# Performance work log

Hardware: AMD Instinct MI355X
Metric: run time of the kernel (lower is better)

Reference implementation:

```python
import jax, jax.numpy as jnp
import numpy as np

SIG = [1, 1, 1, 1, -1]  # Cl(4,1)
NVEC = 5
GA = 1 << NVEC  # 32


def _build_gp_table():
    # Cayley table for the geometric product on blades indexed by bitmask.
    G = np.zeros((GA, GA, GA), np.float32)
    for a in range(GA):
        for b in range(GA):
            s = 0
            t = a >> 1
            while t:
                s += bin(t & b).count('1')
                t >>= 1
            sign = -1.0 if (s & 1) else 1.0
            common = a & b
            for i in range(NVEC):
                if (common >> i) & 1:
                    sign *= SIG[i]
            G[a, b, a ^ b] = sign
    return G

GP_TABLE = jnp.asarray(_build_gp_table())


def geometric_product(x, y):
    return jnp.einsum('...i,...j,ijk->...k', x, y, GP_TABLE)


def manifold_norm(x):
    # normalize each multivector onto the unit sphere in R^32
    return x / (jnp.linalg.norm(x, axis=-1, keepdims=True) + 1e-6)


def versor_linear(x, W, b):
    # channel mixing shared across multivector components: x [..., in, ga]
    return jnp.einsum('...ig,oi->...og', x, W) + b


def layer_norm2d(x, w, b):
    # LayerNorm over last two dims [D, ga] jointly
    mu = jnp.mean(x, axis=(-2, -1), keepdims=True)
    var = jnp.var(x, axis=(-2, -1), keepdims=True)
    return (x - mu) / jnp.sqrt(var + 1e-5) * w + b


def attention(x, Wq, bq, Wk, bk, Wv, bv, Wo, bo, n_heads):
    B, S, D, G = x.shape
    dh = D // n_heads
    q = versor_linear(x, Wq, bq).reshape(B, S, n_heads, dh, G)
    k = versor_linear(x, Wk, bk).reshape(B, S, n_heads, dh, G)
    v = versor_linear(x, Wv, bv).reshape(B, S, n_heads, dh, G)
    scale = 1.0 / np.sqrt(dh * G).astype(np.float32)
    scores = jnp.einsum('bshdg,bthdg->bhst', q, k) * scale
    probs = jax.nn.softmax(scores, axis=-1)
    o = jnp.einsum('bhst,bthdg->bshdg', probs, v).reshape(B, S, D, G)
    return versor_linear(o, Wo, bo)


N_HEADS = 8


def forward(x, Wq, bq, Wk, bk, Wv, bv, Wo, bo, ln1_w, ln1_b, ln2_w, ln2_b,
            gamma1, gamma2, W1, b1, W2, b2, Wr, br, Wc, bc):
    L = Wq.shape[0]
    for l in range(L):
        h = attention(layer_norm2d(x, ln1_w[l], ln1_b[l]),
                      Wq[l], bq[l], Wk[l], bk[l], Wv[l], bv[l], Wo[l], bo[l], N_HEADS)
        x = manifold_norm(x + gamma1[l] * h)
        m = versor_linear(layer_norm2d(x, ln2_w[l], ln2_b[l]), W1[l], b1[l])
        m = versor_linear(jnp.tanh(m), W2[l], b2[l])
        x = manifold_norm(x + gamma2[l] * m)
    # RecursiveRotorAccumulator: log(S)-step inclusive scan of rotors
    delta = versor_linear(x, Wr, br)
    rot = 0.5 * delta
    rot = rot.at[..., 0].add(1.0)
    rot = manifold_norm(rot)
    S = x.shape[1]
    step = 1
    while step < S:
        left = rot[:, :-step]
        right = rot[:, step:]
        comb = manifold_norm(geometric_product(right, left))
        rot = jnp.concatenate([rot[:, :step], comb], axis=1)
        step *= 2
    pooled = rot[:, -1]  # [B, D, ga]
    logits = pooled.reshape(pooled.shape[0], -1) @ Wc.T + bc
    return logits


def setup_inputs() -> dict:
    key = jax.random.key(0)
    B, S, D, G, L, NC = 8, 256, 64, GA, 4, 1000
    E = 4 * D  # expansion hidden
    ks = jax.random.split(key, 16)
    sd = 0.02
    inp = {
        'x': jax.random.normal(ks[0], (B, S, D, G), jnp.float32),
        'Wq': jax.random.normal(ks[1], (L, D, D), jnp.float32) * sd,
        'bq': jnp.zeros((L, D, G), jnp.float32),
        'Wk': jax.random.normal(ks[2], (L, D, D), jnp.float32) * sd,
        'bk': jnp.zeros((L, D, G), jnp.float32),
        'Wv': jax.random.normal(ks[3], (L, D, D), jnp.float32) * sd,
        'bv': jnp.zeros((L, D, G), jnp.float32),
        'Wo': jax.random.normal(ks[4], (L, D, D), jnp.float32) * sd,
        'bo': jnp.zeros((L, D, G), jnp.float32),
        'ln1_w': jnp.ones((L, D, G), jnp.float32),
        'ln1_b': jnp.zeros((L, D, G), jnp.float32),
        'ln2_w': jnp.ones((L, D, G), jnp.float32),
        'ln2_b': jnp.zeros((L, D, G), jnp.float32),
        'gamma1': 1e-5 * jnp.ones((L, D, G), jnp.float32),
        'gamma2': 1e-5 * jnp.ones((L, D, G), jnp.float32),
        'W1': jax.random.normal(ks[5], (L, E, D), jnp.float32) * sd,
        'b1': jnp.zeros((L, E, G), jnp.float32),
        'W2': jax.random.normal(ks[6], (L, D, E), jnp.float32) * sd,
        'b2': jnp.zeros((L, D, G), jnp.float32),
        'Wr': jax.random.normal(ks[7], (D, D), jnp.float32) * sd,
        'br': jnp.zeros((D, G), jnp.float32),
        'Wc': jax.random.normal(ks[8], (NC, D * G), jnp.float32) * sd,
        'bc': jnp.zeros((NC,), jnp.float32),
    }
    return inp


def reference(x, Wq, bq, Wk, bk, Wv, bv, Wo, bo, ln1_w, ln1_b, ln2_w, ln2_b,
              gamma1, gamma2, W1, b1, W2, b2, Wr, br, Wc, bc):
    return forward(x, Wq, bq, Wk, bk, Wv, bv, Wo, bo, ln1_w, ln1_b, ln2_w, ln2_b,
                   gamma1, gamma2, W1, b1, W2, b2, Wr, br, Wc, bc)
```

## Files before the change

kernel.cpp:

```cpp
#include <hip/hip_runtime.h>
#include <hip/hip_bf16.h>

constexpr int kB  = 8;
constexpr int kS  = 256;
constexpr int kD  = 64;
constexpr int kG  = 32;
constexpr int kE  = 256;
constexpr int kNH = 8;
constexpr int kHD = 256;
constexpr int kDG = kD * kG;
constexpr int kT  = kB * kS;
constexpr int kNC = 1000;

using bf16x8 = __attribute__((ext_vector_type(8))) short;
using f32x4  = __attribute__((ext_vector_type(4))) float;

__device__ __forceinline__ short f2bf(float f) {
    unsigned u = __float_as_uint(f);
    unsigned r = (u + 0x7FFFu + ((u >> 16) & 1u)) >> 16;
    return (short)r;
}

__device__ __forceinline__ float tanh_fast(float x) {
    float a = fabsf(x);
    float e = __expf(-2.f * a);
    float t = (1.f - e) / (1.f + e);
    return copysignf(t, x);
}

__global__ __launch_bounds__(256) void ln_kernel(const float* __restrict__ Xin,
                                                 const float* __restrict__ w,
                                                 const float* __restrict__ b,
                                                 float* __restrict__ A) {
    int t = blockIdx.x, tid = threadIdx.x;
    const float* xp = Xin + (size_t)t * kDG;
    __shared__ float r1[256], r2[256];
    float v[8], s = 0.f, ss = 0.f;
#pragma unroll
    for (int j = 0; j < 8; j++) {
        float x = xp[tid + j * 256];
        v[j] = x; s += x; ss += x * x;
    }
    r1[tid] = s; r2[tid] = ss; __syncthreads();
    for (int o = 128; o > 0; o >>= 1) {
        if (tid < o) { r1[tid] += r1[tid + o]; r2[tid] += r2[tid + o]; }
        __syncthreads();
    }
    float mean = r1[0] * (1.f / kDG);
    float var  = r2[0] * (1.f / kDG) - mean * mean;
    float rstd = rsqrtf(var + 1e-5f);
    float* ao = A + (size_t)t * kDG;
#pragma unroll
    for (int j = 0; j < 8; j++) {
        int jj = tid + j * 256;
        ao[jj] = (v[j] - mean) * rstd * w[jj] + b[jj];
    }
}

__device__ __forceinline__ void epi_res_mn_ln(
    const f32x4 (&acc)[4][2], const float* __restrict__ bias,
    const float* __restrict__ Xin, float* __restrict__ Xout,
    const float* __restrict__ gamma,
    const float* __restrict__ lnw, const float* __restrict__ lnb,
    float* __restrict__ Aout, int tok, int l16, int quad, bool do_ln) {
    const size_t tb = (size_t)tok * kDG;
    float xv[4][2][4];
    float s = 0.f, ss = 0.f;
#pragma unroll
    for (int mt = 0; mt < 4; ++mt)
#pragma unroll
        for (int r = 0; r < 4; ++r) {
            int o = mt * 16 + quad * 4 + r;
            float vv[2]; float sq = 0.f;
#pragma unroll
            for (int nt = 0; nt < 2; ++nt) {
                int g = nt * 16 + l16;
                float h = acc[mt][nt][r] + bias[o * kG + g];
                float v = Xin[tb + o * kG + g] + gamma[o * kG + g] * h;
                vv[nt] = v; sq = fmaf(v, v, sq);
            }
#pragma unroll
            for (int off = 1; off < 16; off <<= 1) sq += __shfl_xor(sq, off, 64);
            float rn = 1.f / (sqrtf(sq) + 1e-6f);
#pragma unroll
            for (int nt = 0; nt < 2; ++nt) {
                int g = nt * 16 + l16;
                float x = vv[nt] * rn;
                xv[mt][nt][r] = x;
                Xout[tb + o * kG + g] = x;
                s += x; ss = fmaf(x, x, ss);
            }
        }
    if (!do_ln) return;
#pragma unroll
    for (int off = 1; off < 64; off <<= 1) {
        s += __shfl_xor(s, off, 64); ss += __shfl_xor(ss, off, 64);
    }
    float mean = s * (1.f / kDG);
    float var  = ss * (1.f / kDG) - mean * mean;
    float rstd = rsqrtf(var + 1e-5f);
#pragma unroll
    for (int mt = 0; mt < 4; ++mt)
#pragma unroll
        for (int nt = 0; nt < 2; ++nt) {
            int g = nt * 16 + l16;
#pragma unroll
            for (int r = 0; r < 4; ++r) {
                int o = mt * 16 + quad * 4 + r;
                Aout[tb + o * kG + g] = (xv[mt][nt][r] - mean) * rstd * lnw[o * kG + g] + lnb[o * kG + g];
            }
        }
}

__global__ __launch_bounds__(256) void vlinT_kernel(const float* __restrict__ X,
                                                    const float* __restrict__ W,
                                                    const float* __restrict__ bias,
                                                    float* __restrict__ OutT) {
    __shared__ float sx[kDG];
    __shared__ float sw[kD * kD];
    int t = blockIdx.x, tid = threadIdx.x;
    const float* xp = X + (size_t)t * kDG;
    for (int j = tid; j < kDG; j += 256) sx[j] = xp[j];
    for (int j = tid; j < kD * kD; j += 256) sw[j] = W[j];
    __syncthreads();
    int g = tid & 31, ob = tid >> 5;
    int b = t >> 8, s = t & 255;
    float* op = OutT + ((size_t)b * kD * kS + s) * kG;
    for (int o = ob; o < kD; o += 8) {
        float acc = bias[o * kG + g];
        const float* wr = sw + o * kD;
#pragma unroll
        for (int i = 0; i < kD; i++) acc += wr[i] * sx[i * kG + g];
        op[(size_t)o * kS * kG + g] = acc;
    }
}

__global__ __launch_bounds__(256, 2) void mlp1_kernel(
    const float* __restrict__ X, const float* __restrict__ W,
    const float* __restrict__ bias, unsigned short* __restrict__ outH) {
    constexpr int M = 256;
    constexpr int WS = 64 + 8;
    __shared__ short sW[M * WS];
    __shared__ short sXT[4][32][WS];

    const int tid = threadIdx.x, wave = tid >> 6, lane = tid & 63;
    const int l16 = lane & 15, quad = lane >> 4;
    const int tok = blockIdx.x * 4 + wave;

    for (int j = tid * 4; j < M * 64; j += 1024) {
        const float4 w4 = *(const float4*)(W + j);
        int o = j >> 6, i = j & 63;
        *(short4*)&sW[o * WS + i] = make_short4(f2bf(w4.x), f2bf(w4.y), f2bf(w4.z), f2bf(w4.w));
    }
    {
        const int g4 = (lane & 7) * 4;
        const int i0 = (lane >> 3) * 8;
        const float* xp = X + (size_t)tok * kDG;
#pragma unroll
        for (int half = 0; half < 2; ++half) {
            float4 vr[4];
#pragma unroll
            for (int r = 0; r < 4; ++r)
                vr[r] = *(const float4*)(xp + (i0 + half * 4 + r) * kG + g4);
#pragma unroll
            for (int gg = 0; gg < 4; ++gg)
                *(short4*)&sXT[wave][g4 + gg][i0 + half * 4] =
                    make_short4(f2bf((&vr[0].x)[gg]), f2bf((&vr[1].x)[gg]),
                                f2bf((&vr[2].x)[gg]), f2bf((&vr[3].x)[gg]));
        }
    }
    __syncthreads();

    bf16x8 bfr[2][2];
#pragma unroll
    for (int c = 0; c < 2; ++c)
#pragma unroll
        for (int nt = 0; nt < 2; ++nt)
            bfr[c][nt] = *(const bf16x8*)&sXT[wave][nt * 16 + l16][c * 32 + quad * 8];

    f32x4 acc[16][2];
#pragma unroll
    for (int mt = 0; mt < 16; ++mt)
#pragma unroll
        for (int nt = 0; nt < 2; ++nt) acc[mt][nt] = (f32x4){0.f, 0.f, 0.f, 0.f};

#pragma unroll
    for (int mt = 0; mt < 16; ++mt)
#pragma unroll
        for (int c = 0; c < 2; ++c) {
            bf16x8 afr = *(const bf16x8*)&sW[(mt * 16 + l16) * WS + c * 32 + quad * 8];
#pragma unroll
            for (int nt = 0; nt < 2; ++nt)
                acc[mt][nt] = __builtin_amdgcn_mfma_f32_16x16x32_bf16(afr, bfr[c][nt], acc[mt][nt], 0, 0, 0);
        }

    unsigned short* op = outH + (size_t)tok * M * kG;
#pragma unroll
    for (int mt = 0; mt < 16; ++mt)
#pragma unroll
        for (int nt = 0; nt < 2; ++nt) {
            int g = nt * 16 + l16;
            int e0 = mt * 16 + quad * 4;
            short4 s4;
            s4.x = f2bf(tanh_fast(acc[mt][nt][0] + bias[(e0 + 0) * kG + g]));
            s4.y = f2bf(tanh_fast(acc[mt][nt][1] + bias[(e0 + 1) * kG + g]));
            s4.z = f2bf(tanh_fast(acc[mt][nt][2] + bias[(e0 + 2) * kG + g]));
            s4.w = f2bf(tanh_fast(acc[mt][nt][3] + bias[(e0 + 3) * kG + g]));
            *(short4*)&op[g * M + e0] = s4;
        }
}

__global__ __launch_bounds__(256, 2) void gemmWo_fused_kernel(
    const float* __restrict__ X, const float* __restrict__ W,
    const float* __restrict__ bias,
    const float* __restrict__ Xin, const float* __restrict__ gamma,
    const float* __restrict__ lnw, const float* __restrict__ lnb,
    float* __restrict__ Xout, float* __restrict__ Aout) {
    constexpr int WS = 64 + 8;
    __shared__ short sW[64 * WS];
    __shared__ short sXT[4][32][WS];

    const int tid = threadIdx.x, wave = tid >> 6, lane = tid & 63;
    const int l16 = lane & 15, quad = lane >> 4;
    const int tok = blockIdx.x * 4 + wave;

    for (int j = tid * 4; j < 64 * 64; j += 1024) {
        const float4 w4 = *(const float4*)(W + j);
        int o = j >> 6, i = j & 63;
        *(short4*)&sW[o * WS + i] = make_short4(f2bf(w4.x), f2bf(w4.y), f2bf(w4.z), f2bf(w4.w));
    }
    {
        const int g4 = (lane & 7) * 4;
        const int i0 = (lane >> 3) * 8;
        const float* xp = X + (size_t)tok * kDG;
#pragma unroll
        for (int half = 0; half < 2; ++half) {
            float4 vr[4];
#pragma unroll
            for (int r = 0; r < 4; ++r)
                vr[r] = *(const float4*)(xp + (i0 + half * 4 + r) * kG + g4);
#pragma unroll
            for (int gg = 0; gg < 4; ++gg)
                *(short4*)&sXT[wave][g4 + gg][i0 + half * 4] =
                    make_short4(f2bf((&vr[0].x)[gg]), f2bf((&vr[1].x)[gg]),
                                f2bf((&vr[2].x)[gg]), f2bf((&vr[3].x)[gg]));
        }
    }
    __syncthreads();

    bf16x8 bfr[2][2];
#pragma unroll
    for (int c = 0; c < 2; ++c)
#pragma unroll
        for (int nt = 0; nt < 2; ++nt)
            bfr[c][nt] = *(const bf16x8*)&sXT[wave][nt * 16 + l16][c * 32 + quad * 8];

    f32x4 acc[4][2];
#pragma unroll
    for (int mt = 0; mt < 4; ++mt)
#pragma unroll
        for (int nt = 0; nt < 2; ++nt) acc[mt][nt] = (f32x4){0.f, 0.f, 0.f, 0.f};

#pragma unroll
    for (int mt = 0; mt < 4; ++mt)
#pragma unroll
        for (int c = 0; c < 2; ++c) {
            bf16x8 afr = *(const bf16x8*)&sW[(mt * 16 + l16) * WS + c * 32 + quad * 8];
#pragma unroll
            for (int nt = 0; nt < 2; ++nt)
                acc[mt][nt] = __builtin_amdgcn_mfma_f32_16x16x32_bf16(afr, bfr[c][nt], acc[mt][nt], 0, 0, 0);
        }

    epi_res_mn_ln(acc, bias, Xin, Xout, gamma, lnw, lnb, Aout, tok, l16, quad, true);
}

__global__ __launch_bounds__(256, 2) void gemm_qkv_kernel(
    const float* __restrict__ X,
    const float* __restrict__ Wq, const float* __restrict__ Wk, const float* __restrict__ Wv,
    const float* __restrict__ bq, const float* __restrict__ bk, const float* __restrict__ bv,
    unsigned short* __restrict__ Q, unsigned short* __restrict__ K, unsigned short* __restrict__ V) {
    constexpr int WS = 64 + 8;
    __shared__ short sW[3 * 64 * WS];
    __shared__ short sXT[4][32][WS];

    const int tid = threadIdx.x, wave = tid >> 6, lane = tid & 63;
    const int l16 = lane & 15, quad = lane >> 4;
    const int tok = blockIdx.x * 4 + wave;

    const float* Wp[3] = {Wq, Wk, Wv};
#pragma unroll
    for (int w = 0; w < 3; ++w)
        for (int j = tid * 4; j < 64 * 64; j += 1024) {
            const float4 w4 = *(const float4*)(Wp[w] + j);
            int o = j >> 6, i = j & 63;
            *(short4*)&sW[w * 64 * WS + o * WS + i] =
                make_short4(f2bf(w4.x), f2bf(w4.y), f2bf(w4.z), f2bf(w4.w));
        }
    {
        const int g4 = (lane & 7) * 4;
        const int i0 = (lane >> 3) * 8;
        const float* xp = X + (size_t)tok * kDG;
#pragma unroll
        for (int half = 0; half < 2; ++half) {
            float4 vr[4];
#pragma unroll
            for (int r = 0; r < 4; ++r)
                vr[r] = *(const float4*)(xp + (i0 + half * 4 + r) * kG + g4);
#pragma unroll
            for (int gg = 0; gg < 4; ++gg)
                *(short4*)&sXT[wave][g4 + gg][i0 + half * 4] =
                    make_short4(f2bf((&vr[0].x)[gg]), f2bf((&vr[1].x)[gg]),
                                f2bf((&vr[2].x)[gg]), f2bf((&vr[3].x)[gg]));
        }
    }
    __syncthreads();

    bf16x8 bfr[2][2];
#pragma unroll
    for (int c = 0; c < 2; ++c)
#pragma unroll
        for (int nt = 0; nt < 2; ++nt)
            bfr[c][nt] = *(const bf16x8*)&sXT[wave][nt * 16 + l16][c * 32 + quad * 8];

    f32x4 acc[3][4][2];
#pragma unroll
    for (int w = 0; w < 3; ++w)
#pragma unroll
        for (int mt = 0; mt < 4; ++mt)
#pragma unroll
            for (int nt = 0; nt < 2; ++nt) acc[w][mt][nt] = (f32x4){0.f, 0.f, 0.f, 0.f};

#pragma unroll
    for (int w = 0; w < 3; ++w)
#pragma unroll
        for (int mt = 0; mt < 4; ++mt)
#pragma unroll
            for (int c = 0; c < 2; ++c) {
                bf16x8 afr = *(const bf16x8*)&sW[w * 64 * WS + (mt * 16 + l16) * WS + c * 32 + quad * 8];
#pragma unroll
                for (int nt = 0; nt < 2; ++nt)
                    acc[w][mt][nt] = __builtin_amdgcn_mfma_f32_16x16x32_bf16(afr, bfr[c][nt], acc[w][mt][nt], 0, 0, 0);
            }

    unsigned short* Op[3] = {Q, K, V};
    const float* Bp[3] = {bq, bk, bv};
#pragma unroll
    for (int w = 0; w < 3; ++w) {
        unsigned short* op = Op[w] + (size_t)tok * kDG;
#pragma unroll
        for (int mt = 0; mt < 4; ++mt)
#pragma unroll
            for (int nt = 0; nt < 2; ++nt) {
                int g = nt * 16 + l16;
#pragma unroll
                for (int r = 0; r < 4; ++r) {
                    int o = mt * 16 + quad * 4 + r;
                    op[o * kG + g] = (unsigned short)f2bf(acc[w][mt][nt][r] + Bp[w][o * kG + g]);
                }
            }
    }
}

template<bool DO_LN>
__global__ __launch_bounds__(256, 2) void mlp2_fused_kernel(
    const unsigned short* __restrict__ Mb,
    const float* __restrict__ W2, const float* __restrict__ b2,
    float* __restrict__ X, const float* __restrict__ gamma,
    const float* __restrict__ lnw, const float* __restrict__ lnb,
    float* __restrict__ Aout) {
    constexpr int WS = 256 + 8;
    __shared__ short sW[64 * WS];
    const int tid = threadIdx.x, wave = tid >> 6, lane = tid & 63;
    const int l16 = lane & 15, quad = lane >> 4;
    const int tok = blockIdx.x * 4 + wave;

    for (int j = tid * 4; j < 64 * 256; j += 1024) {
        const float4 w4 = *(const float4*)(W2 + j);
        int o = j >> 8, i = j & 255;
        *(short4*)&sW[o * WS + i] = make_short4(f2bf(w4.x), f2bf(w4.y), f2bf(w4.z), f2bf(w4.w));
    }
    __syncthreads();

    f32x4 acc[4][2];
#pragma unroll
    for (int mt = 0; mt < 4; ++mt)
#pragma unroll
        for (int nt = 0; nt < 2; ++nt) acc[mt][nt] = (f32x4){0.f, 0.f, 0.f, 0.f};

    const unsigned short* mp = Mb + (size_t)tok * kG * kE;
#pragma unroll
    for (int c = 0; c < 8; ++c) {
        bf16x8 bfr[2];
#pragma unroll
        for (int nt = 0; nt < 2; ++nt)
            bfr[nt] = *(const bf16x8*)&mp[(nt * 16 + l16) * kE + c * 32 + quad * 8];
#pragma unroll
        for (int mt = 0; mt < 4; ++mt) {
            bf16x8 afr = *(const bf16x8*)&sW[(mt * 16 + l16) * WS + c * 32 + quad * 8];
#pragma unroll
            for (int nt = 0; nt < 2; ++nt)
                acc[mt][nt] = __builtin_amdgcn_mfma_f32_16x16x32_bf16(afr, bfr[nt], acc[mt][nt], 0, 0, 0);
        }
    }

    epi_res_mn_ln(acc, b2, X, X, gamma, lnw, lnb, Aout, tok, l16, quad, DO_LN);
}

constexpr int QSTR = 264;
constexpr int VSTR = 40;

__global__ __launch_bounds__(256) void attn_mfma_kernel(const unsigned short* __restrict__ Q,
                                                        const unsigned short* __restrict__ K,
                                                        const unsigned short* __restrict__ V,
                                                        float* __restrict__ O) {
    __shared__ short sQ[64 * QSTR];
    __shared__ short sKV[256 * VSTR];

    const int qt = blockIdx.x, h = blockIdx.y, b = blockIdx.z;
    const int tid = threadIdx.x;
    const int wave = tid >> 6, lane = tid & 63;
    const int l16 = lane & 15, quad = lane >> 4;

    const size_t bh = (size_t)b * kS * kDG + (size_t)h * kHD;

#pragma unroll
    for (int it = 0; it < 8; ++it) {
        int j = it * 2048 + tid * 8;
        int row = j >> 8, col = j & 255;
        *(bf16x8*)&sQ[row * QSTR + col] =
            *(const bf16x8*)(Q + bh + (size_t)(qt * 64 + row) * kDG + col);
    }
    __syncthreads();

    bf16x8 afrag[8];
    {
        int row = wave * 16 + l16;
#pragma unroll
        for (int c = 0; c < 8; ++c)
            afrag[c] = *(const bf16x8*)&sQ[row * QSTR + c * 32 + quad * 8];
    }

    f32x4 acc[16];
#pragma unroll
    for (int i = 0; i < 16; ++i) acc[i] = (f32x4){0.f, 0.f, 0.f, 0.f};

    for (int kt = 0; kt < 8; ++kt) {
        __syncthreads();
#pragma unroll
        for (int it = 0; it < 4; ++it) {
            int j = it * 2048 + tid * 8;
            int row = j >> 8, col = j & 255;
            *(bf16x8*)&sKV[row * QSTR + col] =
                *(const bf16x8*)(K + bh + (size_t)(kt * 32 + row) * kDG + col);
        }
        __syncthreads();
#pragma unroll
        for (int nt = 0; nt < 2; ++nt) {
            int key = nt * 16 + l16;
            f32x4 a = acc[kt * 2 + nt];
#pragma unroll
            for (int c = 0; c < 8; ++c) {
                bf16x8 bfrag = *(const bf16x8*)&sKV[key * QSTR + c * 32 + quad * 8];
                a = __builtin_amdgcn_mfma_f32_16x16x32_bf16(afrag[c], bfrag, a, 0, 0, 0);
            }
            acc[kt * 2 + nt] = a;
        }
    }
    __syncthreads();

    float inv[4];
#pragma unroll
    for (int r = 0; r < 4; ++r) {
        float m = -1e30f;
#pragma unroll
        for (int t = 0; t < 16; ++t) m = fmaxf(m, acc[t][r]);
#pragma unroll
        for (int off = 1; off < 16; off <<= 1) m = fmaxf(m, __shfl_xor(m, off, 16));
        float s = 0.f;
#pragma unroll
        for (int t = 0; t < 16; ++t) {
            float p = __expf((acc[t][r] - m) * 0.0625f);
            acc[t][r] = p; s += p;
        }
#pragma unroll
        for (int off = 1; off < 16; off <<= 1) s += __shfl_xor(s, off, 16);
        inv[r] = 1.f / s;
    }

#pragma unroll
    for (int t = 0; t < 16; ++t)
#pragma unroll
        for (int r = 0; r < 4; ++r)
            sQ[(wave * 16 + quad * 4 + r) * QSTR + t * 16 + l16] = f2bf(acc[t][r]);

    f32x4 oacc[16];
#pragma unroll
    for (int i = 0; i < 16; ++i) oacc[i] = (f32x4){0.f, 0.f, 0.f, 0.f};

    for (int vt = 0; vt < 8; ++vt) {
        __syncthreads();
        {
            int kb = tid >> 5;
#pragma unroll
            for (int it = 0; it < 2; ++it) {
                int db = (tid & 31) + it * 32;
                short4 vr[4];
#pragma unroll
                for (int r = 0; r < 4; ++r)
                    vr[r] = *(const short4*)(V + bh + (size_t)(vt * 32 + kb * 4 + r) * kDG + db * 4);
#pragma unroll
                for (int i = 0; i < 4; ++i) {
                    short4 p = make_short4((&vr[0].x)[i], (&vr[1].x)[i],
                                           (&vr[2].x)[i], (&vr[3].x)[i]);
                    *(short4*)&sKV[(db * 4 + i) * VSTR + kb * 4] = p;
                }
            }
        }
        __syncthreads();
        bf16x8 pfrag = *(const bf16x8*)&sQ[(wave * 16 + l16) * QSTR + vt * 32 + quad * 8];
#pragma unroll
        for (int dt = 0; dt < 16; ++dt) {
            bf16x8 vfrag = *(const bf16x8*)&sKV[(dt * 16 + l16) * VSTR + quad * 8];
            oacc[dt] = __builtin_amdgcn_mfma_f32_16x16x32_bf16(pfrag, vfrag, oacc[dt], 0, 0, 0);
        }
    }

    {
        int qrow = qt * 64 + wave * 16 + quad * 4;
#pragma unroll
        for (int dt = 0; dt < 16; ++dt)
#pragma unroll
            for (int r = 0; r < 4; ++r)
                O[bh + (size_t)(qrow + r) * kDG + dt * 16 + l16] = oacc[dt][r] * inv[r];
    }
}

constexpr int pc_ce(unsigned v) { int c = 0; while (v) { c += v & 1; v >>= 1; } return c; }
constexpr unsigned gp_mask_ce(int a) {
    unsigned m = 0;
    for (int c = 0; c < 32; ++c) {
        int b = a ^ c;
        int s = (a & b) >> 4;
        for (int t = a >> 1; t; t >>= 1) s += pc_ce(t & b);
        if (s & 1) m |= (1u << c);
    }
    return m;
}

template<int A>
__device__ __forceinline__ void gp_term(const float* x, const float* y, float* acc) {
    constexpr unsigned m = gp_mask_ce(A);
    const float xa = x[A], nxa = -xa;
#pragma unroll
    for (int c = 0; c < 32; ++c)
        acc[c] = fmaf(((m >> c) & 1u) ? nxa : xa, y[A ^ c], acc[c]);
}

__device__ __forceinline__ void gp_mn_t(const float* x, const float* y, float* out) {
    float acc[32];
#pragma unroll
    for (int c = 0; c < 32; ++c) acc[c] = 0.f;
    gp_term<0>(x, y, acc);  gp_term<1>(x, y, acc);  gp_term<2>(x, y, acc);  gp_term<3>(x, y, acc);
    gp_term<4>(x, y, acc);  gp_term<5>(x, y, acc);  gp_term<6>(x, y, acc);  gp_term<7>(x, y, acc);
    gp_term<8>(x, y, acc);  gp_term<9>(x, y, acc);  gp_term<10>(x, y, acc); gp_term<11>(x, y, acc);
    gp_term<12>(x, y, acc); gp_term<13>(x, y, acc); gp_term<14>(x, y, acc); gp_term<15>(x, y, acc);
    gp_term<16>(x, y, acc); gp_term<17>(x, y, acc); gp_term<18>(x, y, acc); gp_term<19>(x, y, acc);
    gp_term<20>(x, y, acc); gp_term<21>(x, y, acc); gp_term<22>(x, y, acc); gp_term<23>(x, y, acc);
    gp_term<24>(x, y, acc); gp_term<25>(x, y, acc); gp_term<26>(x, y, acc); gp_term<27>(x, y, acc);
    gp_term<28>(x, y, acc); gp_term<29>(x, y, acc); gp_term<30>(x, y, acc); gp_term<31>(x, y, acc);
    float ss = 0.f;
#pragma unroll
    for (int c = 0; c < 32; ++c) ss = fmaf(acc[c], acc[c], ss);
    float r = 1.f / (sqrtf(ss) + 1e-6f);
#pragma unroll
    for (int c = 0; c < 32; ++c) out[c] = acc[c] * r;
}

__device__ __forceinline__ void leaf_load(const float* base, float* v) {
#pragma unroll
    for (int i = 0; i < 8; ++i) {
        const float4 f = *(const float4*)(base + i * 4);
        v[i * 4 + 0] = 0.5f * f.x; v[i * 4 + 1] = 0.5f * f.y;
        v[i * 4 + 2] = 0.5f * f.z; v[i * 4 + 3] = 0.5f * f.w;
    }
    v[0] += 1.f;
    float ss = 0.f;
#pragma unroll
    for (int c = 0; c < 32; ++c) ss = fmaf(v[c], v[c], ss);
    float r = 1.f / (sqrtf(ss) + 1e-6f);
#pragma unroll
    for (int c = 0; c < 32; ++c) v[c] *= r;
}

__global__ __launch_bounds__(256) void scanreg_kernel(const float* __restrict__ DT,
                                                      float* __restrict__ pooled) {
    const int wave = threadIdx.x >> 6, lane = threadIdx.x & 63;
    const int seq = blockIdx.x * 4 + wave;
    const float* base = DT + ((size_t)seq * kS + lane * 4) * kG;

    float R[32], Y[32], P[32], Xa[32], Yb[32];

    leaf_load(base, R);
    for (int j = 1; j < 4; ++j) {
        leaf_load(base + j * kG, Y);
        gp_mn_t(Y, R, R);
    }

    for (int step = 1; step < 64; step <<= 1) {
        const bool up = lane & step;
#pragma unroll
        for (int c = 0; c < 32; ++c) P[c] = __shfl_xor(R[c], step, 64);
#pragma unroll
        for (int c = 0; c < 32; ++c) {
            Xa[c] = up ? R[c] : P[c];
            Yb[c] = up ? P[c] : R[c];
        }
        gp_mn_t(Xa, Yb, R);
    }

    if (lane == 0) {
        float* op = pooled + (size_t)seq * kG;
#pragma unroll
        for (int i = 0; i < 8; ++i)
            *(float4*)(op + i * 4) = make_float4(R[i * 4], R[i * 4 + 1], R[i * 4 + 2], R[i * 4 + 3]);
    }
}

__global__ __launch_bounds__(256) void cls2_kernel(const float* __restrict__ P,
                                                   const float* __restrict__ Wc,
                                                   const float* __restrict__ bc,
                                                   float* __restrict__ out) {
    __shared__ float sp[kB * kDG];
    const int tid = threadIdx.x, wave = tid >> 6, lane = tid & 63;
    for (int j = tid * 4; j < kB * kDG; j += 1024)
        *(float4*)&sp[j] = *(const float4*)(P + j);
    __syncthreads();

    const int c = blockIdx.x * 4 + wave;
    const float* w = Wc + (size_t)c * kDG;
    float acc[kB];
#pragma unroll
    for (int b = 0; b < kB; ++b) acc[b] = 0.f;
#pragma unroll
    for (int cc = 0; cc < 8; ++cc) {
        const float4 w4 = *(const float4*)(w + cc * 256 + lane * 4);
#pragma unroll
        for (int b = 0; b < kB; ++b) {
            const float4 p4 = *(const float4*)&sp[b * kDG + cc * 256 + lane * 4];
            acc[b] += w4.x * p4.x + w4.y * p4.y + w4.z * p4.z + w4.w * p4.w;
        }
    }
#pragma unroll
    for (int b = 0; b < kB; ++b)
#pragma unroll
        for (int off = 32; off > 0; off >>= 1) acc[b] += __shfl_xor(acc[b], off, 64);
    if (lane == 0) {
        float bias = bc[c];
#pragma unroll
        for (int b = 0; b < kB; ++b) out[b * kNC + c] = acc[b] + bias;
    }
}

extern "C" void kernel_launch(void* const* d_in, const int* in_sizes, int n_in,
                              void* d_out, int out_size, void* d_ws, size_t ws_size,
                              hipStream_t stream) {
    const float* x_in = (const float*)d_in[0];
    const float* Wq   = (const float*)d_in[1];
    const float* bq   = (const float*)d_in[2];
    const float* Wk   = (const float*)d_in[3];
    const float* bk   = (const float*)d_in[4];
    const float* Wv   = (const float*)d_in[5];
    const float* bv   = (const float*)d_in[6];
    const float* Wo   = (const float*)d_in[7];
    const float* bo   = (const float*)d_in[8];
    const float* ln1w = (const float*)d_in[9];
    const float* ln1b = (const float*)d_in[10];
    const float* ln2w = (const float*)d_in[11];
    const float* ln2b = (const float*)d_in[12];
    const float* gm1  = (const float*)d_in[13];
    const float* gm2  = (const float*)d_in[14];
    const float* W1   = (const float*)d_in[15];
    const float* b1   = (const float*)d_in[16];
    const float* W2   = (const float*)d_in[17];
    const float* b2   = (const float*)d_in[18];
    const float* Wr   = (const float*)d_in[19];
    const float* br   = (const float*)d_in[20];
    const float* Wc   = (const float*)d_in[21];
    const float* bc   = (const float*)d_in[22];

    const size_t NEL = (size_t)kT * kDG;
    float* F  = (float*)d_ws;
    float* X  = F;
    float* A  = F + NEL;
    float* Qb = F + 2 * NEL;
    float* Kb = F + 3 * NEL;
    float* Vb = F + 4 * NEL;
    unsigned short* Qh = (unsigned short*)Qb;
    unsigned short* Kh = (unsigned short*)Kb;
    unsigned short* Vh = (unsigned short*)Vb;
    unsigned short* Mb = (unsigned short*)Kb;
    float* pooled = Qb;

    ln_kernel<<<kT, 256, 0, stream>>>(x_in, ln1w, ln1b, A);

    for (int l = 0; l < 4; l++) {
        gemm_qkv_kernel<<<kT / 4, 256, 0, stream>>>(A,
            Wq + l * kD * kD, Wk + l * kD * kD, Wv + l * kD * kD,
            bq + l * kDG, bk + l * kDG, bv + l * kDG, Qh, Kh, Vh);
        attn_mfma_kernel<<<dim3(4, kNH, kB), 256, 0, stream>>>(Qh, Kh, Vh, A);
        gemmWo_fused_kernel<<<kT / 4, 256, 0, stream>>>(A, Wo + l * kD * kD, bo + l * kDG,
            l == 0 ? x_in : X, gm1 + l * kDG, ln2w + l * kDG, ln2b + l * kDG, X, A);
        mlp1_kernel<<<kT / 4, 256, 0, stream>>>(A, W1 + l * kE * kD, b1 + l * kE * kG, Mb);
        if (l < 3)
            mlp2_fused_kernel<true><<<kT / 4, 256, 0, stream>>>(Mb, W2 + l * kD * kE, b2 + l * kDG,
                X, gm2 + l * kDG, ln1w + (l + 1) * kDG, ln1b + (l + 1) * kDG, A);
        else
            mlp2_fused_kernel<false><<<kT / 4, 256, 0, stream>>>(Mb, W2 + l * kD * kE, b2 + l * kDG,
                X, gm2 + l * kDG, nullptr, nullptr, nullptr);
    }

    vlinT_kernel<<<kT, 256, 0, stream>>>(X, Wr, br, A);
    scanreg_kernel<<<kB * kD / 4, 256, 0, stream>>>(A, pooled);
    cls2_kernel<<<kNC / 4, 256, 0, stream>>>(pooled, Wc, bc, (float*)d_out);
}
```

Measured before the change: 610.6 us.

## Pre-convert weights to bf16 once and register-prefetch K/V tiles in attention

Adds a single up-front kernel that converts all layer weights (Wq, Wk, Wv, Wo, W1, W2) to bf16 in a workspace buffer. Each GEMM block then copies ready-made bf16 weights into shared memory instead of re-reading fp32 and converting in every one of the 512 blocks per launch. In the attention kernel, the next K and V tile is loaded into registers while the current tile is being computed, and barriers are rearranged to overlap global loads with MFMA work. This raises register pressure and uses extra workspace memory.

```diff
diff --git a/kernel.cpp b/kernel.cpp
--- a/kernel.cpp
+++ b/kernel.cpp
@@ -26,6 +26,23 @@
     float e = __expf(-2.f * a);
     float t = (1.f - e) / (1.f + e);
     return copysignf(t, x);
+}
+
+__global__ __launch_bounds__(256) void cvtw_kernel(
+    const float* __restrict__ Wq, const float* __restrict__ Wk,
+    const float* __restrict__ Wv, const float* __restrict__ Wo,
+    const float* __restrict__ W1, const float* __restrict__ W2,
+    unsigned short* __restrict__ dst) {
+    int idx = (blockIdx.x * 256 + threadIdx.x) * 4;
+    const float* src; int off;
+    if      (idx <  16384) { src = Wq; off = 0; }
+    else if (idx <  32768) { src = Wk; off = 16384; }
+    else if (idx <  49152) { src = Wv; off = 32768; }
+    else if (idx <  65536) { src = Wo; off = 49152; }
+    else if (idx < 131072) { src = W1; off = 65536; }
+    else                   { src = W2; off = 131072; }
+    const float4 v = *(const float4*)(src + (idx - off));
+    *(short4*)&dst[idx] = make_short4(f2bf(v.x), f2bf(v.y), f2bf(v.z), f2bf(v.w));
 }
 
 __global__ __launch_bounds__(256) void ln_kernel(const float* __restrict__ Xin,
@@ -136,7 +153,7 @@
 }
 
 __global__ __launch_bounds__(256, 2) void mlp1_kernel(
-    const float* __restrict__ X, const float* __restrict__ W,
+    const float* __restrict__ X, const unsigned short* __restrict__ Wh,
     const float* __restrict__ bias, unsigned short* __restrict__ outH) {
     constexpr int M = 256;
     constexpr int WS = 64 + 8;
@@ -147,10 +164,9 @@
     const int l16 = lane & 15, quad = lane >> 4;
     const int tok = blockIdx.x * 4 + wave;
 
-    for (int j = tid * 4; j < M * 64; j += 1024) {
-        const float4 w4 = *(const float4*)(W + j);
+    for (int j = tid * 8; j < M * 64; j += 2048) {
         int o = j >> 6, i = j & 63;
-        *(short4*)&sW[o * WS + i] = make_short4(f2bf(w4.x), f2bf(w4.y), f2bf(w4.z), f2bf(w4.w));
+        *(bf16x8*)&sW[o * WS + i] = *(const bf16x8*)(Wh + j);
     }
     {
         const int g4 = (lane & 7) * 4;
@@ -211,7 +227,7 @@
 }
 
 __global__ __launch_bounds__(256, 2) void gemmWo_fused_kernel(
-    const float* __restrict__ X, const float* __restrict__ W,
+    const float* __restrict__ X, const unsigned short* __restrict__ Wh,
     const float* __restrict__ bias,
     const float* __restrict__ Xin, const float* __restrict__ gamma,
     const float* __restrict__ lnw, const float* __restrict__ lnb,
@@ -224,10 +240,9 @@
     const int l16 = lane & 15, quad = lane >> 4;
     const int tok = blockIdx.x * 4 + wave;
 
-    for (int j = tid * 4; j < 64 * 64; j += 1024) {
-        const float4 w4 = *(const float4*)(W + j);
+    for (int j = tid * 8; j < 64 * 64; j += 2048) {
         int o = j >> 6, i = j & 63;
-        *(short4*)&sW[o * WS + i] = make_short4(f2bf(w4.x), f2bf(w4.y), f2bf(w4.z), f2bf(w4.w));
+        *(bf16x8*)&sW[o * WS + i] = *(const bf16x8*)(Wh + j);
     }
     {
         const int g4 = (lane & 7) * 4;
@@ -276,7 +291,8 @@
 
 __global__ __launch_bounds__(256, 2) void gemm_qkv_kernel(
     const float* __restrict__ X,
-    const float* __restrict__ Wq, const float* __restrict__ Wk, const float* __restrict__ Wv,
+    const unsigned short* __restrict__ Wqh, const unsigned short* __restrict__ Wkh,
+    const unsigned short* __restrict__ Wvh,
     const float* __restrict__ bq, const float* __restrict__ bk, const float* __restrict__ bv,
     unsigned short* __restrict__ Q, unsigned short* __restrict__ K, unsigned short* __restrict__ V) {
     constexpr int WS = 64 + 8;
@@ -287,14 +303,12 @@
     const int l16 = lane & 15, quad = lane >> 4;
     const int tok = blockIdx.x * 4 + wave;
 
-    const float* Wp[3] = {Wq, Wk, Wv};
+    const unsigned short* Wp[3] = {Wqh, Wkh, Wvh};
 #pragma unroll
     for (int w = 0; w < 3; ++w)
-        for (int j = tid * 4; j < 64 * 64; j += 1024) {
-            const float4 w4 = *(const float4*)(Wp[w] + j);
+        for (int j = tid * 8; j < 64 * 64; j += 2048) {
             int o = j >> 6, i = j & 63;
-            *(short4*)&sW[w * 64 * WS + o * WS + i] =
-                make_short4(f2bf(w4.x), f2bf(w4.y), f2bf(w4.z), f2bf(w4.w));
+            *(bf16x8*)&sW[w * 64 * WS + o * WS + i] = *(const bf16x8*)(Wp[w] + j);
         }
     {
         const int g4 = (lane & 7) * 4;
@@ -364,7 +378,7 @@
 template<bool DO_LN>
 __global__ __launch_bounds__(256, 2) void mlp2_fused_kernel(
     const unsigned short* __restrict__ Mb,
-    const float* __restrict__ W2, const float* __restrict__ b2,
+    const unsigned short* __restrict__ W2h, const float* __restrict__ b2,
     float* __restrict__ X, const float* __restrict__ gamma,
     const float* __restrict__ lnw, const float* __restrict__ lnb,
     float* __restrict__ Aout) {
@@ -374,10 +388,9 @@
     const int l16 = lane & 15, quad = lane >> 4;
     const int tok = blockIdx.x * 4 + wave;
 
-    for (int j = tid * 4; j < 64 * 256; j += 1024) {
-        const float4 w4 = *(const float4*)(W2 + j);
+    for (int j = tid * 8; j < 64 * 256; j += 2048) {
         int o = j >> 8, i = j & 255;
-        *(short4*)&sW[o * WS + i] = make_short4(f2bf(w4.x), f2bf(w4.y), f2bf(w4.z), f2bf(w4.w));
+        *(bf16x8*)&sW[o * WS + i] = *(const bf16x8*)(W2h + j);
     }
     __syncthreads();
 
@@ -430,6 +443,13 @@
         *(bf16x8*)&sQ[row * QSTR + col] =
             *(const bf16x8*)(Q + bh + (size_t)(qt * 64 + row) * kDG + col);
     }
+    bf16x8 kpre[4];
+#pragma unroll
+    for (int it = 0; it < 4; ++it) {
+        int j = it * 2048 + tid * 8;
+        int row = j >> 8, col = j & 255;
+        kpre[it] = *(const bf16x8*)(K + bh + (size_t)row * kDG + col);
+    }
     __syncthreads();
 
     bf16x8 afrag[8];
@@ -445,15 +465,21 @@
     for (int i = 0; i < 16; ++i) acc[i] = (f32x4){0.f, 0.f, 0.f, 0.f};
 
     for (int kt = 0; kt < 8; ++kt) {
-        __syncthreads();
 #pragma unroll
         for (int it = 0; it < 4; ++it) {
             int j = it * 2048 + tid * 8;
             int row = j >> 8, col = j & 255;
-            *(bf16x8*)&sKV[row * QSTR + col] =
-                *(const bf16x8*)(K + bh + (size_t)(kt * 32 + row) * kDG + col);
+            *(bf16x8*)&sKV[row * QSTR + col] = kpre[it];
         }
         __syncthreads();
+        if (kt < 7) {
+#pragma unroll
+            for (int it = 0; it < 4; ++it) {
+                int j = it * 2048 + tid * 8;
+                int row = j >> 8, col = j & 255;
+                kpre[it] = *(const bf16x8*)(K + bh + (size_t)((kt + 1) * 32 + row) * kDG + col);
+            }
+        }
 #pragma unroll
         for (int nt = 0; nt < 2; ++nt) {
             int key = nt * 16 + l16;
@@ -465,8 +491,8 @@
             }
             acc[kt * 2 + nt] = a;
         }
-    }
-    __syncthreads();
+        __syncthreads();
+    }
 
     float inv[4];
 #pragma unroll
@@ -492,6 +518,18 @@
 #pragma unroll
         for (int r = 0; r < 4; ++r)
             sQ[(wave * 16 + quad * 4 + r) * QSTR + t * 16 + l16] = f2bf(acc[t][r]);
+
+    short4 vpre[8];
+    {
+        int kb = tid >> 5;
+#pragma unroll
+        for (int it = 0; it < 2; ++it) {
+            int db = (tid & 31) + it * 32;
+#pragma unroll
+            for (int r = 0; r < 4; ++r)
+                vpre[it * 4 + r] = *(const short4*)(V + bh + (size_t)(kb * 4 + r) * kDG + db * 4);
+        }
+    }
 
     f32x4 oacc[16];
 #pragma unroll
@@ -504,19 +542,25 @@
 #pragma unroll
             for (int it = 0; it < 2; ++it) {
                 int db = (tid & 31) + it * 32;
-                short4 vr[4];
-#pragma unroll
-                for (int r = 0; r < 4; ++r)
-                    vr[r] = *(const short4*)(V + bh + (size_t)(vt * 32 + kb * 4 + r) * kDG + db * 4);
 #pragma unroll
                 for (int i = 0; i < 4; ++i) {
-                    short4 p = make_short4((&vr[0].x)[i], (&vr[1].x)[i],
-                                           (&vr[2].x)[i], (&vr[3].x)[i]);
+                    short4 p = make_short4((&vpre[it * 4 + 0].x)[i], (&vpre[it * 4 + 1].x)[i],
+                                           (&vpre[it * 4 + 2].x)[i], (&vpre[it * 4 + 3].x)[i]);
                     *(short4*)&sKV[(db * 4 + i) * VSTR + kb * 4] = p;
                 }
             }
         }
         __syncthreads();
+        if (vt < 7) {
+            int kb = tid >> 5;
+#pragma unroll
+            for (int it = 0; it < 2; ++it) {
+                int db = (tid & 31) + it * 32;
+#pragma unroll
+                for (int r = 0; r < 4; ++r)
+                    vpre[it * 4 + r] = *(const short4*)(V + bh + (size_t)((vt + 1) * 32 + kb * 4 + r) * kDG + db * 4);
+            }
+        }
         bf16x8 pfrag = *(const bf16x8*)&sQ[(wave * 16 + l16) * QSTR + vt * 32 + quad * 8];
 #pragma unroll
         for (int dt = 0; dt < 16; ++dt) {
@@ -692,34 +736,41 @@
     float* F  = (float*)d_ws;
     float* X  = F;
     float* A  = F + NEL;
-    float* Qb = F + 2 * NEL;
-    float* Kb = F + 3 * NEL;
-    float* Vb = F + 4 * NEL;
-    unsigned short* Qh = (unsigned short*)Qb;
-    unsigned short* Kh = (unsigned short*)Kb;
-    unsigned short* Vh = (unsigned short*)Vb;
-    unsigned short* Mb = (unsigned short*)Kb;
-    float* pooled = Qb;
+    unsigned short* Qh = (unsigned short*)(F + 2 * NEL);
+    unsigned short* Kh = (unsigned short*)(F + 3 * NEL);
+    unsigned short* Vh = (unsigned short*)(F + 4 * NEL);
+    unsigned short* Mb = (unsigned short*)(F + 3 * NEL);
+    unsigned short* Wb = (unsigned short*)(F + 5 * NEL);
+    float* pooled = F + 2 * NEL;
+    float* DT = A;
+
+    cvtw_kernel<<<192, 256, 0, stream>>>(Wq, Wk, Wv, Wo, W1, W2, Wb);
+    unsigned short* Wqh = Wb;
+    unsigned short* Wkh = Wb + 16384;
+    unsigned short* Wvh = Wb + 32768;
+    unsigned short* Woh = Wb + 49152;
+    unsigned short* W1h = Wb + 65536;
+    unsigned short* W2h = Wb + 131072;
 
     ln_kernel<<<kT, 256, 0, stream>>>(x_in, ln1w, ln1b, A);
 
     for (int l = 0; l < 4; l++) {
         gemm_qkv_kernel<<<kT / 4, 256, 0, stream>>>(A,
-            Wq + l * kD * kD, Wk + l * kD * kD, Wv + l * kD * kD,
+            Wqh + l * 4096, Wkh + l * 4096, Wvh + l * 4096,
             bq + l * kDG, bk + l * kDG, bv + l * kDG, Qh, Kh, Vh);
         attn_mfma_kernel<<<dim3(4, kNH, kB), 256, 0, stream>>>(Qh, Kh, Vh, A);
-        gemmWo_fused_kernel<<<kT / 4, 256, 0, stream>>>(A, Wo + l * kD * kD, bo + l * kDG,
+        gemmWo_fused_kernel<<<kT / 4, 256, 0, stream>>>(A, Woh + l * 4096, bo + l * kDG,
             l == 0 ? x_in : X, gm1 + l * kDG, ln2w + l * kDG, ln2b + l * kDG, X, A);
-        mlp1_kernel<<<kT / 4, 256, 0, stream>>>(A, W1 + l * kE * kD, b1 + l * kE * kG, Mb);
+        mlp1_kernel<<<kT / 4, 256, 0, stream>>>(A, W1h + l * 16384, b1 + l * kE * kG, Mb);
         if (l < 3)
-            mlp2_fused_kernel<true><<<kT / 4, 256, 0, stream>>>(Mb, W2 + l * kD * kE, b2 + l * kDG,
+            mlp2_fused_kernel<true><<<kT / 4, 256, 0, stream>>>(Mb, W2h + l * 16384, b2 + l * kDG,
                 X, gm2 + l * kDG, ln1w + (l + 1) * kDG, ln1b + (l + 1) * kDG, A);
         else
-            mlp2_fused_kernel<false><<<kT / 4, 256, 0, stream>>>(Mb, W2 + l * kD * kE, b2 + l * kDG,
+            mlp2_fused_kernel<false><<<kT / 4, 256, 0, stream>>>(Mb, W2h + l * 16384, b2 + l * kDG,
                 X, gm2 + l * kDG, nullptr, nullptr, nullptr);
     }
 
-    vlinT_kernel<<<kT, 256, 0, stream>>>(X, Wr, br, A);
-    scanreg_kernel<<<kB * kD / 4, 256, 0, stream>>>(A, pooled);
+    vlinT_kernel<<<kT, 256, 0, stream>>>(X, Wr, br, DT);
+    scanreg_kernel<<<kB * kD / 4, 256, 0, stream>>>(DT, pooled);
     cls2_kernel<<<kNC / 4, 256, 0, stream>>>(pooled, Wc, bc, (float*)d_out);
 }
```

Measured after the change: 560.6 us. 1.09x faster.
